# Kernel tuning notes

Hardware: AMD Instinct MI355X
Metric: run time of the kernel (lower is better)

Reference implementation:

```python
import math
import jax, jax.numpy as jnp
import numpy as np

# dims: batch, in-channels, out-channels, features (freq bins), frames, heads, expansion
B, C, CO, F, W, NH, EXP = 1, 8, 8, 512, 256, 8, 4
CC = C + CO          # channels into cross-attn query (cat of h and self_attn)
FC = C + 2 * CO      # channels into FFN (cat of h, self_attn, src_attn)
FH = F * EXP         # FFN hidden features


def mc_linear(x, pw, dw=None):
    # x: [B,Cin,Fin,W]; pw: [Cin,Fout,Fin] per-channel positionwise matmul;
    # dw: [Cout,Cin] channel-mixing matmul ('depthwise' in the repo's naming)
    y = jnp.einsum('bcfw,cgf->bcgw', x, pw)
    if dw is not None:
        y = jnp.einsum('bcgw,oc->bogw', y, dw)
    return y


def frame_conv(x, w, b):
    # Conv2d kernel (1,3), padding (0,1): 1D conv along the frame axis
    y = jax.lax.conv_general_dilated(x, w, (1, 1), ((0, 0), (1, 1)),
                                     dimension_numbers=('NCHW', 'OIHW', 'NCHW'))
    return y + b[None, :, None, None]


def mc_layernorm(x, g, b, eps=1e-5):
    # normalize over the feature axis (2), per (batch, channel, frame)
    mu = x.mean(axis=2, keepdims=True)
    var = jnp.mean(jnp.square(x - mu), axis=2, keepdims=True)
    return (x - mu) * jax.lax.rsqrt(var + eps) * g[None, :, :, None] + b[None, :, :, None]


def mc_attention(xq, xkv, q_pw, q_dw, q_cw, q_cb, k_pw, k_cw, k_cb, v_pw, v_cw, v_cb, o_pw):
    q = frame_conv(mc_linear(xq, q_pw, q_dw), q_cw, q_cb)   # [B,CO,F,Wq]
    k = frame_conv(mc_linear(xkv, k_pw), k_cw, k_cb)        # [B,CO,F,Wk]
    v = frame_conv(mc_linear(xkv, v_pw), v_cw, v_cb)
    dh = F // NH

    def heads(t):  # [B,CO,F,Wt] -> [B,CO,NH,Wt,dh]
        b_, c_, f_, w_ = t.shape
        return t.transpose(0, 1, 3, 2).reshape(b_, c_, w_, NH, dh).transpose(0, 1, 3, 2, 4)

    qh, kh, vh = heads(q), heads(k), heads(v)
    qk = jnp.einsum('bchqd,bchkd->bchqk', qh, kh) / math.sqrt(F)
    a = jnp.einsum('bchqk,bchkd->bchqd', jax.nn.softmax(qk, axis=-1), vh)
    b_, c_, h_, w_, _ = a.shape
    a = a.transpose(0, 1, 3, 2, 4).reshape(b_, c_, w_, F).transpose(0, 1, 3, 2)  # [B,CO,F,Wq]
    return mc_linear(a, o_pw), qk


def setup_inputs() -> dict:
    key = jax.random.key(0)
    ks = jax.random.split(key, 32)
    it = iter(range(32))

    def rn(shape, s=0.02):
        return jax.random.normal(ks[next(it)], shape, jnp.float32) * s

    inp = {
        'x': jax.random.normal(ks[next(it)], (B, C, F, W), jnp.float32),
        'src': jax.random.normal(ks[next(it)], (B, C, F, W), jnp.float32),
        'ln_g': jnp.ones((C, F), jnp.float32),
        'ln_b': jnp.zeros((C, F), jnp.float32),
        # self-attention (C -> CO, C == CO so no channel-mix on projections)
        'sa_q_pw': rn((C, F, F)), 'sa_q_cw': rn((CO, CO, 1, 3), 0.1), 'sa_q_cb': jnp.zeros((CO,), jnp.float32),
        'sa_k_pw': rn((C, F, F)), 'sa_k_cw': rn((CO, CO, 1, 3), 0.1), 'sa_k_cb': jnp.zeros((CO,), jnp.float32),
        'sa_v_pw': rn((C, F, F)), 'sa_v_cw': rn((CO, CO, 1, 3), 0.1), 'sa_v_cb': jnp.zeros((CO,), jnp.float32),
        'sa_o_pw': rn((CO, F, F)),
        # cross-attention (query from CC=C+CO channels -> CO; key/value from src with C channels)
        'ca_q_pw': rn((CC, F, F)), 'ca_q_dw': rn((CO, CC), 0.1),
        'ca_q_cw': rn((CO, CO, 1, 3), 0.1), 'ca_q_cb': jnp.zeros((CO,), jnp.float32),
        'ca_k_pw': rn((C, F, F)), 'ca_k_cw': rn((CO, CO, 1, 3), 0.1), 'ca_k_cb': jnp.zeros((CO,), jnp.float32),
        'ca_v_pw': rn((C, F, F)), 'ca_v_cw': rn((CO, CO, 1, 3), 0.1), 'ca_v_cb': jnp.zeros((CO,), jnp.float32),
        'ca_o_pw': rn((CO, F, F)),
        # FFN
        'ffn1_pw': rn((FC, FH, F)), 'ffn1_dw': rn((FC, FC), 0.1),
        'ffn2_pw': rn((FC, F, FH)), 'ffn2_dw': rn((C, FC), 0.1),
    }
    return inp


def reference(x, src, ln_g, ln_b,
              sa_q_pw, sa_q_cw, sa_q_cb, sa_k_pw, sa_k_cw, sa_k_cb, sa_v_pw, sa_v_cw, sa_v_cb, sa_o_pw,
              ca_q_pw, ca_q_dw, ca_q_cw, ca_q_cb, ca_k_pw, ca_k_cw, ca_k_cb, ca_v_pw, ca_v_cw, ca_v_cb, ca_o_pw,
              ffn1_pw, ffn1_dw, ffn2_pw, ffn2_dw):
    h = mc_layernorm(x, ln_g, ln_b)
    sa, qk1 = mc_attention(h, h, sa_q_pw, None, sa_q_cw, sa_q_cb,
                           sa_k_pw, sa_k_cw, sa_k_cb, sa_v_pw, sa_v_cw, sa_v_cb, sa_o_pw)
    ca, qk2 = mc_attention(jnp.concatenate([h, sa], axis=1), src,
                           ca_q_pw, ca_q_dw, ca_q_cw, ca_q_cb,
                           ca_k_pw, ca_k_cw, ca_k_cb, ca_v_pw, ca_v_cw, ca_v_cb, ca_o_pw)
    z = mc_linear(jnp.concatenate([h, sa, ca], axis=1), ffn1_pw, ffn1_dw)
    z = jax.nn.gelu(z, approximate=False)
    z = mc_linear(z, ffn2_pw, ffn2_dw)
    return (x + z, qk1, qk2)
```

## Files before the change

### kernel.cpp

```cpp
#include <hip/hip_runtime.h>
#include <math.h>

typedef __attribute__((ext_vector_type(4))) float f32x4;
typedef __attribute__((ext_vector_type(8))) short s16x8;
typedef __attribute__((ext_vector_type(4))) short s16x4;

__device__ __forceinline__ unsigned short f2b(float f) {
    union { float f; unsigned u; } v; v.f = f;
    unsigned r = v.u + 0x7fffu + ((v.u >> 16) & 1u);
    return (unsigned short)(r >> 16);
}
__device__ __forceinline__ float b2f(unsigned short u) {
    union { unsigned u; float f; } v; v.u = ((unsigned)u) << 16;
    return v.f;
}

constexpr int kF = 512;
constexpr int kW = 256;
constexpr int kFW = kF * kW;

__global__ __launch_bounds__(256) void ln_t_kernel(const float* __restrict__ x,
                                                   const float* __restrict__ g,
                                                   const float* __restrict__ b,
                                                   unsigned short* __restrict__ hTb) {
    int c = blockIdx.x >> 4;
    int w0 = (blockIdx.x & 15) * 16;
    int t = threadIdx.x;
    int wi = t & 15, fg = t >> 4;
    const float* xb = x + (size_t)c * kFW + w0 + wi;
    float sum = 0.f, sum2 = 0.f;
    for (int j = 0; j < 32; ++j) {
        float v = xb[(size_t)(fg * 32 + j) * kW];
        sum += v; sum2 += v * v;
    }
    __shared__ float s1[16][16], s2[16][16];
    s1[fg][wi] = sum; s2[fg][wi] = sum2;
    __syncthreads();
    float ts = 0.f, tq = 0.f;
    #pragma unroll
    for (int j = 0; j < 16; ++j) { ts += s1[j][wi]; tq += s2[j][wi]; }
    float mu = ts * (1.0f / 512.0f);
    float rstd = rsqrtf(tq * (1.0f / 512.0f) - mu * mu + 1e-5f);
    const float* gc = g + c * kF + fg * 32;
    const float* bc = b + c * kF + fg * 32;
    unsigned short* ob = hTb + (size_t)c * kFW + (size_t)(w0 + wi) * kF + fg * 32;
    for (int j = 0; j < 32; j += 4) {
        float v0 = xb[(size_t)(fg * 32 + j + 0) * kW];
        float v1 = xb[(size_t)(fg * 32 + j + 1) * kW];
        float v2 = xb[(size_t)(fg * 32 + j + 2) * kW];
        float v3 = xb[(size_t)(fg * 32 + j + 3) * kW];
        s16x4 p = { (short)f2b((v0 - mu) * rstd * gc[j + 0] + bc[j + 0]),
                    (short)f2b((v1 - mu) * rstd * gc[j + 1] + bc[j + 1]),
                    (short)f2b((v2 - mu) * rstd * gc[j + 2] + bc[j + 2]),
                    (short)f2b((v3 - mu) * rstd * gc[j + 3] + bc[j + 3]) };
        *(s16x4*)(&ob[j]) = p;
    }
}

__global__ __launch_bounds__(256) void tcvt_kernel(const float* __restrict__ in,
                                                   unsigned short* __restrict__ out) {
    int c = blockIdx.x, f0 = blockIdx.y * 64, w0 = blockIdx.z * 64;
    __shared__ float tile[64][65];
    int t = threadIdx.x;
    int tw = t & 63, tf4 = t >> 6;
    for (int i = 0; i < 16; ++i) {
        int f = tf4 * 16 + i;
        tile[f][tw] = in[(size_t)c * kFW + (size_t)(f0 + f) * kW + w0 + tw];
    }
    __syncthreads();
    int w = t >> 2, fc = (t & 3) * 16;
    unsigned short* ob = out + (size_t)c * kFW + (size_t)(w0 + w) * kF + f0 + fc;
    for (int j = 0; j < 16; j += 4) {
        s16x4 p = { (short)f2b(tile[fc + j + 0][w]), (short)f2b(tile[fc + j + 1][w]),
                    (short)f2b(tile[fc + j + 2][w]), (short)f2b(tile[fc + j + 3][w]) };
        *(s16x4*)(&ob[j]) = p;
    }
}

struct WSeg { const float* A; const unsigned short* B; void* C; int omode; };
struct WB5 { WSeg s[5]; };

__global__ __launch_bounds__(256) void wgemm256(WB5 wb, int M, int K, int Klocal,
                                                long a_ch, long b_ch, long c_ch, long c_split,
                                                int segshift, int nm, int ksplit) {
    __shared__ unsigned short lds[16384];
    int t = threadIdx.x, lane = t & 63, wv = t >> 6;
    int l16 = lane & 15, l4 = lane >> 4;

    int id = blockIdx.x;
    int r = id & 7, j = id >> 3;
    int per = nm * ksplit;
    int y = r + 8 * (j / per);
    int rem = j % per;
    int mt = rem % nm;
    int kz = rem / nm;
    int seg = y >> segshift, c = y & ((1 << segshift) - 1);
    WSeg sg = wb.s[seg];
    int bm = mt * 64;
    int kbase = kz * Klocal;

    const float* A = sg.A + (size_t)c * a_ch + kbase;
    const unsigned short* B = sg.B + (size_t)c * b_ch + kbase;
    const float* arow = A + (size_t)(bm + wv * 16 + l16) * K + l4 * 8;

    int srow = t >> 3, sck = t & 7;
    const unsigned short* bsrc = B + (size_t)srow * K + sck * 8;
    unsigned short* sdst = &lds[srow * 64 + ((sck * 8) ^ ((srow & 7) << 3))];

    s16x8 stg0, stg1, stg2, stg3, stg4, stg5, stg6, stg7;
    #define LOADSTG(c0) do { \
        const unsigned short* _b = bsrc + (size_t)(c0) * 64; \
        stg0 = *(const s16x8*)(_b); \
        stg1 = *(const s16x8*)(_b + (size_t)32 * K); \
        stg2 = *(const s16x8*)(_b + (size_t)64 * K); \
        stg3 = *(const s16x8*)(_b + (size_t)96 * K); \
        stg4 = *(const s16x8*)(_b + (size_t)128 * K); \
        stg5 = *(const s16x8*)(_b + (size_t)160 * K); \
        stg6 = *(const s16x8*)(_b + (size_t)192 * K); \
        stg7 = *(const s16x8*)(_b + (size_t)224 * K); \
    } while (0)
    #define WRITESTG() do { \
        *(s16x8*)(&sdst[0])     = stg0; \
        *(s16x8*)(&sdst[2048])  = stg1; \
        *(s16x8*)(&sdst[4096])  = stg2; \
        *(s16x8*)(&sdst[6144])  = stg3; \
        *(s16x8*)(&sdst[8192])  = stg4; \
        *(s16x8*)(&sdst[10240]) = stg5; \
        *(s16x8*)(&sdst[12288]) = stg6; \
        *(s16x8*)(&sdst[14336]) = stg7; \
    } while (0)

    f32x4 acc[16];
    #pragma unroll
    for (int i = 0; i < 16; ++i) acc[i] = (f32x4){0.f, 0.f, 0.f, 0.f};

    LOADSTG(0);
    WRITESTG();

    f32x4 pa0 = __builtin_nontemporal_load((const f32x4*)arow);
    f32x4 pa1 = __builtin_nontemporal_load((const f32x4*)(arow + 4));

    int nc = Klocal >> 6;
    for (int cch = 0; cch < nc; ++cch) {
        __syncthreads();
        if (cch + 1 < nc) LOADSTG(cch + 1);
        #pragma unroll
        for (int ks = 0; ks < 2; ++ks) {
            f32x4 c0 = pa0, c1 = pa1;
            int nk = cch * 64 + (ks + 1) * 32;
            if (nk < Klocal) {
                pa0 = __builtin_nontemporal_load((const f32x4*)(arow + nk));
                pa1 = __builtin_nontemporal_load((const f32x4*)(arow + nk + 4));
            }
            s16x8 af = { (short)f2b(c0.x), (short)f2b(c0.y), (short)f2b(c0.z), (short)f2b(c0.w),
                         (short)f2b(c1.x), (short)f2b(c1.y), (short)f2b(c1.z), (short)f2b(c1.w) };
            #pragma unroll
            for (int ni = 0; ni < 16; ++ni) {
                int rr = ni * 16 + l16;
                s16x8 bf = *(const s16x8*)(&lds[rr * 64 + (((ks * 32 + l4 * 8)) ^ ((rr & 7) << 3))]);
                acc[ni] = __builtin_amdgcn_mfma_f32_16x16x32_bf16(af, bf, acc[ni], 0, 0, 0);
            }
        }
        __syncthreads();
        if (cch + 1 < nc) WRITESTG();
    }
    #undef LOADSTG
    #undef WRITESTG

    int m0 = bm + wv * 16 + l4 * 4;
    if (sg.omode == 2) {
        unsigned short* C = (unsigned short*)sg.C + (size_t)c * c_ch;
        #pragma unroll
        for (int ni = 0; ni < 16; ++ni) {
            int n = ni * 16 + l16;
            s16x4 pk = { (short)f2b(acc[ni][0]), (short)f2b(acc[ni][1]),
                         (short)f2b(acc[ni][2]), (short)f2b(acc[ni][3]) };
            *(s16x4*)(&C[(size_t)n * M + m0]) = pk;
        }
    } else if (sg.omode == 1) {
        unsigned short* C = (unsigned short*)sg.C + (size_t)c * c_ch;
        #pragma unroll
        for (int ni = 0; ni < 16; ++ni) {
            int n = ni * 16 + l16;
            #pragma unroll
            for (int rr = 0; rr < 4; ++rr)
                C[(size_t)(m0 + rr) * 256 + n] = f2b(acc[ni][rr]);
        }
    } else {
        float* C = (float*)sg.C + (size_t)c * c_ch + (size_t)kz * c_split;
        #pragma unroll
        for (int ni = 0; ni < 16; ++ni) {
            int n = ni * 16 + l16;
            #pragma unroll
            for (int rr = 0; rr < 4; ++rr)
                C[(size_t)(m0 + rr) * 256 + n] = acc[ni][rr];
        }
    }
}

template<int OMODE, int BN>
__global__ __launch_bounds__(256) void gemm_mfma(
    const unsigned short* __restrict__ Av, const unsigned short* __restrict__ B,
    void* __restrict__ Cv,
    int M, int N, int K,
    long a_hi, long a_lo, long b_hi, long b_lo, long c_hi, long c_lo,
    int bshift, int a_rs, int b_rs, int c_rs, float scale)
{
    constexpr int NF = BN / 64;
    constexpr int WN = BN / 4;
    __shared__ unsigned char lds[8192 + BN * 128];

    int t = threadIdx.x;
    int lane = t & 63, wv = t >> 6;
    int l16 = lane & 15, l4 = lane >> 4;
    int swz = (lane & 7) << 4;

    int by = blockIdx.y;
    int bhi = by >> bshift, blo = by & ((1 << bshift) - 1);
    int ntiles = N / BN;
    int bm = (blockIdx.x / ntiles) * 64;
    int bn = (blockIdx.x % ntiles) * BN;

    const unsigned short* Bp = B + (size_t)bhi * b_hi + (size_t)blo * b_lo + (size_t)bn * b_rs;
    const unsigned short* A = Av + (size_t)bhi * a_hi + (size_t)blo * a_lo;

    f32x4 acc[4][NF];
    #pragma unroll
    for (int i = 0; i < 4; ++i)
        #pragma unroll
        for (int j = 0; j < NF; ++j) acc[i][j] = (f32x4){0.f, 0.f, 0.f, 0.f};

    for (int k0 = 0; k0 < K; k0 += 64) {
        #pragma unroll
        for (int it = 0; it < 2; ++it) {
            int idx = it * 256 + t;
            int rr = idx >> 3, ck = idx & 7;
            s16x8 v = *(const s16x8*)(A + (size_t)(bm + rr) * a_rs + k0 + ck * 8);
            int off = rr * 128 + ((ck * 16) ^ ((rr & 7) << 4));
            *(s16x8*)(&lds[off]) = v;
        }
        #pragma unroll
        for (int it = 0; it < BN / 32; ++it) {
            int idx = it * 256 + t;
            int rr = idx >> 3, ck = idx & 7;
            s16x8 v = *(const s16x8*)(Bp + (size_t)rr * b_rs + k0 + ck * 8);
            int off = 8192 + rr * 128 + ((ck * 16) ^ ((rr & 7) << 4));
            *(s16x8*)(&lds[off]) = v;
        }
        __syncthreads();
        #pragma unroll
        for (int ks = 0; ks < 2; ++ks) {
            s16x8 af[4], bfr[NF];
            #pragma unroll
            for (int mi = 0; mi < 4; ++mi)
                af[mi] = *(const s16x8*)(&lds[(mi * 16 + l16) * 128 + ((ks * 64 + l4 * 16) ^ swz)]);
            #pragma unroll
            for (int ni = 0; ni < NF; ++ni)
                bfr[ni] = *(const s16x8*)(&lds[8192 + (wv * WN + ni * 16 + l16) * 128 + ((ks * 64 + l4 * 16) ^ swz)]);
            #pragma unroll
            for (int mi = 0; mi < 4; ++mi)
                #pragma unroll
                for (int ni = 0; ni < NF; ++ni)
                    acc[mi][ni] = __builtin_amdgcn_mfma_f32_16x16x32_bf16(af[mi], bfr[ni], acc[mi][ni], 0, 0, 0);
        }
        __syncthreads();
    }

    unsigned short* C = (unsigned short*)Cv + (size_t)bhi * c_hi + (size_t)blo * c_lo;
    #pragma unroll
    for (int mi = 0; mi < 4; ++mi)
        #pragma unroll
        for (int ni = 0; ni < NF; ++ni) {
            int n = bn + wv * WN + ni * 16 + l16;
            int m0 = bm + mi * 16 + l4 * 4;
            #pragma unroll
            for (int rr = 0; rr < 4; ++rr)
                C[(size_t)(m0 + rr) * c_rs + n] = f2b(acc[mi][ni][rr] * scale);
        }
}

struct ConvArgs {
    const unsigned short* in[5];
    unsigned short* out[5];
    const float* cw[5];
    const float* cb[5];
    int mode[5];
};

__global__ __launch_bounds__(256) void conv5_kernel(ConvArgs a) {
    int g = blockIdx.y;
    __shared__ float scw[192]; __shared__ float scb[8];
    int t = threadIdx.x;
    if (t < 192) scw[t] = a.cw[g][t];
    if (t >= 192 && t < 200) scb[t - 192] = a.cb[g][t - 192];
    __syncthreads();
    const unsigned short* in = a.in[g];
    unsigned short* out = a.out[g];
    int gi = blockIdx.x * 256 + t;
    int mode = a.mode[g];
    int w = mode ? (gi & 255) : (gi >> 9);
    int str = mode ? 1 : 512;
    float acc[8];
    #pragma unroll
    for (int o = 0; o < 8; ++o) acc[o] = scb[o];
    bool hm = w > 0, hp = w < 255;
    #pragma unroll
    for (int i = 0; i < 8; ++i) {
        size_t base = (size_t)i * kFW + gi;
        float xm = hm ? b2f(in[base - str]) : 0.f;
        float x0 = b2f(in[base]);
        float xp = hp ? b2f(in[base + str]) : 0.f;
        #pragma unroll
        for (int o = 0; o < 8; ++o) {
            const float* wp = &scw[(o * 8 + i) * 3];
            acc[o] += wp[0] * xm + wp[1] * x0 + wp[2] * xp;
        }
    }
    #pragma unroll
    for (int o = 0; o < 8; ++o) out[(size_t)o * kFW + gi] = f2b(acc[o]);
}

__global__ __launch_bounds__(256) void mixconv_kernel(const unsigned short* __restrict__ in,
                                                      const float* __restrict__ dw,
                                                      const float* __restrict__ cw,
                                                      const float* __restrict__ cb,
                                                      unsigned short* __restrict__ out) {
    __shared__ float sdw[128], scw[192], scb[8];
    int t = threadIdx.x;
    if (t < 128) sdw[t] = dw[t];
    if (t >= 128 && t < 136) scb[t - 128] = cb[t - 128];
    if (t < 192) scw[t] = cw[t];
    __syncthreads();
    int gi = blockIdx.x * 256 + t;
    int w = gi >> 9;
    bool hm = w > 0, hp = w < 255;
    float xc[16], xm[16], xp[16];
    #pragma unroll
    for (int cc = 0; cc < 16; ++cc) {
        size_t base = (size_t)cc * kFW + gi;
        xc[cc] = b2f(in[base]);
        xm[cc] = hm ? b2f(in[base - 512]) : 0.f;
        xp[cc] = hp ? b2f(in[base + 512]) : 0.f;
    }
    float mm[8], m0[8], mp[8];
    #pragma unroll
    for (int o = 0; o < 8; ++o) {
        float am = 0.f, a0 = 0.f, ap = 0.f;
        #pragma unroll
        for (int cc = 0; cc < 16; ++cc) {
            float wv = sdw[o * 16 + cc];
            am += wv * xm[cc]; a0 += wv * xc[cc]; ap += wv * xp[cc];
        }
        mm[o] = am; m0[o] = a0; mp[o] = ap;
    }
    #pragma unroll
    for (int o = 0; o < 8; ++o) {
        float acc = scb[o];
        #pragma unroll
        for (int i = 0; i < 8; ++i) {
            const float* wp = &scw[(o * 8 + i) * 3];
            acc += wp[0] * mm[i] + wp[1] * m0[i] + wp[2] * mp[i];
        }
        out[(size_t)o * kFW + gi] = f2b(acc);
    }
}

__global__ __launch_bounds__(256) void qk_softmax_kernel(
    const unsigned short* __restrict__ Qt, const unsigned short* __restrict__ Kt,
    float* __restrict__ S, unsigned short* __restrict__ P, float scale)
{
    __shared__ unsigned char lds[40960];
    __shared__ float smax[4][64];
    __shared__ float ssum[4][64];
    int t = threadIdx.x, lane = t & 63, wv = t >> 6;
    int l16 = lane & 15, l4 = lane >> 4;
    int swz = (lane & 7) << 4;
    int ch = blockIdx.y, c = ch >> 3, h = ch & 7;
    int bm = blockIdx.x * 64;
    const unsigned short* Qb = Qt + (size_t)c * kFW + h * 64;
    const unsigned short* Kb = Kt + (size_t)c * kFW + h * 64;
    float* Sb = S + (size_t)ch * 65536;
    unsigned short* Pb = P + (size_t)ch * 65536;

    #pragma unroll
    for (int it = 0; it < 2; ++it) {
        int idx = it * 256 + t; int rr = idx >> 3, ck = idx & 7;
        s16x8 v = *(const s16x8*)(Qb + (size_t)(bm + rr) * 512 + ck * 8);
        *(s16x8*)(&lds[rr * 128 + ((ck * 16) ^ ((rr & 7) << 4))]) = v;
    }
    #pragma unroll
    for (int it = 0; it < 8; ++it) {
        int idx = it * 256 + t; int rr = idx >> 3, ck = idx & 7;
        s16x8 v = *(const s16x8*)(Kb + (size_t)rr * 512 + ck * 8);
        *(s16x8*)(&lds[8192 + rr * 128 + ((ck * 16) ^ ((rr & 7) << 4))]) = v;
    }
    __syncthreads();
    f32x4 acc[4][4];
    #pragma unroll
    for (int i = 0; i < 4; ++i)
        #pragma unroll
        for (int j = 0; j < 4; ++j) acc[i][j] = (f32x4){0.f, 0.f, 0.f, 0.f};
    #pragma unroll
    for (int ks = 0; ks < 2; ++ks) {
        s16x8 af[4], bfr[4];
        #pragma unroll
        for (int mi = 0; mi < 4; ++mi)
            af[mi] = *(const s16x8*)(&lds[(mi * 16 + l16) * 128 + ((ks * 64 + l4 * 16) ^ swz)]);
        #pragma unroll
        for (int ni = 0; ni < 4; ++ni)
            bfr[ni] = *(const s16x8*)(&lds[8192 + (wv * 64 + ni * 16 + l16) * 128 + ((ks * 64 + l4 * 16) ^ swz)]);
        #pragma unroll
        for (int mi = 0; mi < 4; ++mi)
            #pragma unroll
            for (int ni = 0; ni < 4; ++ni)
                acc[mi][ni] = __builtin_amdgcn_mfma_f32_16x16x32_bf16(af[mi], bfr[ni], acc[mi][ni], 0, 0, 0);
    }
    #pragma unroll
    for (int mi = 0; mi < 4; ++mi)
        #pragma unroll
        for (int ni = 0; ni < 4; ++ni) {
            acc[mi][ni] *= scale;
            int col = wv * 64 + ni * 16 + l16;
            int row0 = bm + mi * 16 + l4 * 4;
            #pragma unroll
            for (int rr = 0; rr < 4; ++rr)
                Sb[(size_t)(row0 + rr) * 256 + col] = acc[mi][ni][rr];
        }
    float rmax[4][4];
    #pragma unroll
    for (int mi = 0; mi < 4; ++mi)
        #pragma unroll
        for (int rr = 0; rr < 4; ++rr)
            rmax[mi][rr] = fmaxf(fmaxf(acc[mi][0][rr], acc[mi][1][rr]), fmaxf(acc[mi][2][rr], acc[mi][3][rr]));
    #pragma unroll
    for (int d = 1; d < 16; d <<= 1)
        #pragma unroll
        for (int mi = 0; mi < 4; ++mi)
            #pragma unroll
            for (int rr = 0; rr < 4; ++rr)
                rmax[mi][rr] = fmaxf(rmax[mi][rr], __shfl_xor(rmax[mi][rr], d));
    if (l16 == 0)
        #pragma unroll
        for (int mi = 0; mi < 4; ++mi)
            #pragma unroll
            for (int rr = 0; rr < 4; ++rr)
                smax[wv][mi * 16 + l4 * 4 + rr] = rmax[mi][rr];
    __syncthreads();
    float rM[4][4], rsum[4][4];
    #pragma unroll
    for (int mi = 0; mi < 4; ++mi)
        #pragma unroll
        for (int rr = 0; rr < 4; ++rr) {
            int row = mi * 16 + l4 * 4 + rr;
            rM[mi][rr] = fmaxf(fmaxf(smax[0][row], smax[1][row]), fmaxf(smax[2][row], smax[3][row]));
            rsum[mi][rr] = 0.f;
        }
    #pragma unroll
    for (int mi = 0; mi < 4; ++mi)
        #pragma unroll
        for (int ni = 0; ni < 4; ++ni)
            #pragma unroll
            for (int rr = 0; rr < 4; ++rr) {
                float e = __expf(acc[mi][ni][rr] - rM[mi][rr]);
                acc[mi][ni][rr] = e;
                rsum[mi][rr] += e;
            }
    #pragma unroll
    for (int d = 1; d < 16; d <<= 1)
        #pragma unroll
        for (int mi = 0; mi < 4; ++mi)
            #pragma unroll
            for (int rr = 0; rr < 4; ++rr)
                rsum[mi][rr] += __shfl_xor(rsum[mi][rr], d);
    if (l16 == 0)
        #pragma unroll
        for (int mi = 0; mi < 4; ++mi)
            #pragma unroll
            for (int rr = 0; rr < 4; ++rr)
                ssum[wv][mi * 16 + l4 * 4 + rr] = rsum[mi][rr];
    __syncthreads();
    #pragma unroll
    for (int mi = 0; mi < 4; ++mi)
        #pragma unroll
        for (int rr = 0; rr < 4; ++rr) {
            int row = mi * 16 + l4 * 4 + rr;
            float inv = 1.f / (ssum[0][row] + ssum[1][row] + ssum[2][row] + ssum[3][row]);
            #pragma unroll
            for (int ni = 0; ni < 4; ++ni)
                Pb[(size_t)(bm + row) * 256 + wv * 64 + ni * 16 + l16] = f2b(acc[mi][ni][rr] * inv);
        }
}

__global__ __launch_bounds__(256) void gelu24_kernel(unsigned short* __restrict__ z,
                                                     const float* __restrict__ dw) {
    __shared__ float sdw[576];
    int t = threadIdx.x;
    for (int i = t; i < 576; i += 256) sdw[i] = dw[i];
    __syncthreads();
    size_t gi = (size_t)blockIdx.x * 256 + t;
    const size_t CH = (size_t)256 * 2048;
    float xv[24];
    #pragma unroll
    for (int cc = 0; cc < 24; ++cc) xv[cc] = b2f(z[cc * CH + gi]);
    #pragma unroll
    for (int o = 0; o < 24; ++o) {
        float s = 0.f;
        #pragma unroll
        for (int cc = 0; cc < 24; ++cc) s += sdw[o * 24 + cc] * xv[cc];
        s = 0.5f * s * (1.0f + erff(s * 0.7071067811865475f));
        z[o * CH + gi] = f2b(s);
    }
}

__global__ __launch_bounds__(256) void final_mix_add2(const float* __restrict__ x,
                                                      const float* __restrict__ z2,
                                                      const float* __restrict__ dw,
                                                      float* __restrict__ out) {
    __shared__ float sdw[192];
    int t = threadIdx.x;
    if (t < 192) sdw[t] = dw[t];
    __syncthreads();
    int gi = blockIdx.x * 256 + t;
    const size_t PSZ = (size_t)24 * kFW;
    float xv[24];
    #pragma unroll
    for (int cc = 0; cc < 24; ++cc) {
        size_t o = (size_t)cc * kFW + gi;
        xv[cc] = z2[o] + z2[PSZ + o];
    }
    #pragma unroll
    for (int o = 0; o < 8; ++o) {
        float s = 0.f;
        #pragma unroll
        for (int cc = 0; cc < 24; ++cc) s += sdw[o * 24 + cc] * xv[cc];
        out[(size_t)o * kFW + gi] = x[(size_t)o * kFW + gi] + s;
    }
}

extern "C" void kernel_launch(void* const* d_in, const int* in_sizes, int n_in,
                              void* d_out, int out_size, void* d_ws, size_t ws_size,
                              hipStream_t stream) {
    const float* x       = (const float*)d_in[0];
    const float* src     = (const float*)d_in[1];
    const float* ln_g    = (const float*)d_in[2];
    const float* ln_b    = (const float*)d_in[3];
    const float* sa_q_pw = (const float*)d_in[4];
    const float* sa_q_cw = (const float*)d_in[5];
    const float* sa_q_cb = (const float*)d_in[6];
    const float* sa_k_pw = (const float*)d_in[7];
    const float* sa_k_cw = (const float*)d_in[8];
    const float* sa_k_cb = (const float*)d_in[9];
    const float* sa_v_pw = (const float*)d_in[10];
    const float* sa_v_cw = (const float*)d_in[11];
    const float* sa_v_cb = (const float*)d_in[12];
    const float* sa_o_pw = (const float*)d_in[13];
    const float* ca_q_pw = (const float*)d_in[14];
    const float* ca_q_dw = (const float*)d_in[15];
    const float* ca_q_cw = (const float*)d_in[16];
    const float* ca_q_cb = (const float*)d_in[17];
    const float* ca_k_pw = (const float*)d_in[18];
    const float* ca_k_cw = (const float*)d_in[19];
    const float* ca_k_cb = (const float*)d_in[20];
    const float* ca_v_pw = (const float*)d_in[21];
    const float* ca_v_cw = (const float*)d_in[22];
    const float* ca_v_cb = (const float*)d_in[23];
    const float* ca_o_pw = (const float*)d_in[24];
    const float* ffn1_pw = (const float*)d_in[25];
    const float* ffn1_dw = (const float*)d_in[26];
    const float* ffn2_pw = (const float*)d_in[27];
    const float* ffn2_dw = (const float*)d_in[28];

    float* out  = (float*)d_out;
    float* qk1o = out + 1048576;
    float* qk2o = out + 1048576 + 4194304;

    unsigned char* ws = (unsigned char*)d_ws;
    unsigned short* CAT24  = (unsigned short*)(ws + 0);
    unsigned short* hTb    = CAT24;
    unsigned short* saTb   = CAT24 + 8 * (size_t)kFW;
    unsigned short* caTb   = CAT24 + 16 * (size_t)kFW;
    unsigned short* SRCT   = (unsigned short*)(ws + 6291456);
    unsigned short* preQ   = (unsigned short*)(ws + 8388608);
    unsigned short* preK   = (unsigned short*)(ws + 10485760);
    unsigned short* preVsa = (unsigned short*)(ws + 12582912);
    unsigned short* preKca = (unsigned short*)(ws + 14680064);
    unsigned short* preVca = (unsigned short*)(ws + 16777216);
    unsigned short* QT     = (unsigned short*)(ws + 18874368);
    unsigned short* KT     = (unsigned short*)(ws + 20971520);
    unsigned short* VNsa   = (unsigned short*)(ws + 23068672);
    unsigned short* KTca   = (unsigned short*)(ws + 25165824);
    unsigned short* VNca   = (unsigned short*)(ws + 27262976);
    unsigned short* PRE16  = (unsigned short*)(ws + 29360128);
    unsigned short* QTca   = (unsigned short*)(ws + 33554432);
    unsigned short* ATTT   = (unsigned short*)(ws + 35651584);
    unsigned short* PB     = (unsigned short*)(ws + 37748736);
    unsigned short* Z0T    = (unsigned short*)(ws + 8388608);
    float*          Z2P    = (float*)(ws + 33554432);

    const float qscale = 0.044194173824159216f;
    dim3 blk(256);

    ln_t_kernel<<<128, blk, 0, stream>>>(x, ln_g, ln_b, hTb);
    tcvt_kernel<<<dim3(8, 8, 4), blk, 0, stream>>>(src, SRCT);

    WB5 p5;
    p5.s[0] = { sa_q_pw, hTb,  preQ,   2 };
    p5.s[1] = { sa_k_pw, hTb,  preK,   2 };
    p5.s[2] = { sa_v_pw, hTb,  preVsa, 1 };
    p5.s[3] = { ca_k_pw, SRCT, preKca, 2 };
    p5.s[4] = { ca_v_pw, SRCT, preVca, 1 };
    wgemm256<<<dim3(320), blk, 0, stream>>>(p5, 512, 512, 512, 262144, kFW, kFW, 0, 3, 8, 1);

    ConvArgs c5;
    c5.in[0] = preQ;   c5.out[0] = QT;   c5.cw[0] = sa_q_cw; c5.cb[0] = sa_q_cb; c5.mode[0] = 0;
    c5.in[1] = preK;   c5.out[1] = KT;   c5.cw[1] = sa_k_cw; c5.cb[1] = sa_k_cb; c5.mode[1] = 0;
    c5.in[2] = preVsa; c5.out[2] = VNsa; c5.cw[2] = sa_v_cw; c5.cb[2] = sa_v_cb; c5.mode[2] = 1;
    c5.in[3] = preKca; c5.out[3] = KTca; c5.cw[3] = ca_k_cw; c5.cb[3] = ca_k_cb; c5.mode[3] = 0;
    c5.in[4] = preVca; c5.out[4] = VNca; c5.cw[4] = ca_v_cw; c5.cb[4] = ca_v_cb; c5.mode[4] = 1;
    conv5_kernel<<<dim3(512, 5), blk, 0, stream>>>(c5);

    qk_softmax_kernel<<<dim3(4, 64), blk, 0, stream>>>(QT, KT, qk1o, PB, qscale);
    gemm_mfma<1, 64><<<dim3(4, 64), blk, 0, stream>>>(PB, VNsa, ATTT, 256, 64, 256,
        524288, 65536, kFW, 16384, kFW, 64, 3, 256, 256, 512, 1.0f);
    WB5 so;
    so.s[0] = { sa_o_pw, ATTT, saTb, 2 };
    so.s[1] = so.s[0]; so.s[2] = so.s[0]; so.s[3] = so.s[0]; so.s[4] = so.s[0];
    wgemm256<<<dim3(64), blk, 0, stream>>>(so, 512, 512, 512, 262144, kFW, kFW, 0, 8, 8, 1);

    WB5 cq;
    cq.s[0] = { ca_q_pw, CAT24, PRE16, 2 };
    cq.s[1] = cq.s[0]; cq.s[2] = cq.s[0]; cq.s[3] = cq.s[0]; cq.s[4] = cq.s[0];
    wgemm256<<<dim3(128), blk, 0, stream>>>(cq, 512, 512, 512, 262144, kFW, kFW, 0, 8, 8, 1);
    mixconv_kernel<<<512, blk, 0, stream>>>(PRE16, ca_q_dw, ca_q_cw, ca_q_cb, QTca);

    qk_softmax_kernel<<<dim3(4, 64), blk, 0, stream>>>(QTca, KTca, qk2o, PB, qscale);
    gemm_mfma<1, 64><<<dim3(4, 64), blk, 0, stream>>>(PB, VNca, ATTT, 256, 64, 256,
        524288, 65536, kFW, 16384, kFW, 64, 3, 256, 256, 512, 1.0f);
    WB5 co;
    co.s[0] = { ca_o_pw, ATTT, caTb, 2 };
    co.s[1] = co.s[0]; co.s[2] = co.s[0]; co.s[3] = co.s[0]; co.s[4] = co.s[0];
    wgemm256<<<dim3(64), blk, 0, stream>>>(co, 512, 512, 512, 262144, kFW, kFW, 0, 8, 8, 1);

    WB5 f1;
    f1.s[0] = { ffn1_pw, CAT24, Z0T, 2 };
    f1.s[1] = f1.s[0]; f1.s[2] = f1.s[0]; f1.s[3] = f1.s[0]; f1.s[4] = f1.s[0];
    wgemm256<<<dim3(768), blk, 0, stream>>>(f1, 2048, 512, 512, 1048576, kFW, 524288, 0, 8, 32, 1);
    gelu24_kernel<<<2048, blk, 0, stream>>>(Z0T, ffn1_dw);
    WB5 f2;
    f2.s[0] = { ffn2_pw, Z0T, Z2P, 0 };
    f2.s[1] = f2.s[0]; f2.s[2] = f2.s[0]; f2.s[3] = f2.s[0]; f2.s[4] = f2.s[0];
    wgemm256<<<dim3(384), blk, 0, stream>>>(f2, 512, 2048, 1024, 1048576, 524288, kFW, 3145728, 8, 8, 2);
    final_mix_add2<<<512, blk, 0, stream>>>(x, Z2P, ffn2_dw, out);
}
```

Measured before the change: 288.4 us.

## Fuse attention kernels, double-buffer weight GEMM, merge prep and early cross-attn Q projection

Combines several changes. LayerNorm and the src transpose now run in one prep launch. The weight GEMM gets double-buffered LDS with A-operand prefetch. QK-softmax and PV are fused into one attention kernel, so the probability matrix no longer round-trips through global memory. The h-part of the cross-attention Q projection moves into the first batched GEMM, so only the sa-part runs later. This cuts launches and intermediate traffic but doubles GEMM LDS usage, which may lower occupancy.

```diff
diff --git a/kernel.cpp b/kernel.cpp
--- a/kernel.cpp
+++ b/kernel.cpp
@@ -19,71 +19,95 @@
 constexpr int kW = 256;
 constexpr int kFW = kF * kW;
 
-__global__ __launch_bounds__(256) void ln_t_kernel(const float* __restrict__ x,
+__global__ __launch_bounds__(256) void prep_kernel(const float* __restrict__ x,
                                                    const float* __restrict__ g,
                                                    const float* __restrict__ b,
-                                                   unsigned short* __restrict__ hTb) {
-    int c = blockIdx.x >> 4;
-    int w0 = (blockIdx.x & 15) * 16;
+                                                   unsigned short* __restrict__ hTb,
+                                                   const float* __restrict__ src,
+                                                   unsigned short* __restrict__ SRCT) {
+    __shared__ float tile[64][65];
+    __shared__ float s1[16][16], s2[16][16];
+    int bid = blockIdx.x;
     int t = threadIdx.x;
-    int wi = t & 15, fg = t >> 4;
-    const float* xb = x + (size_t)c * kFW + w0 + wi;
-    float sum = 0.f, sum2 = 0.f;
-    for (int j = 0; j < 32; ++j) {
-        float v = xb[(size_t)(fg * 32 + j) * kW];
-        sum += v; sum2 += v * v;
-    }
-    __shared__ float s1[16][16], s2[16][16];
-    s1[fg][wi] = sum; s2[fg][wi] = sum2;
-    __syncthreads();
-    float ts = 0.f, tq = 0.f;
-    #pragma unroll
-    for (int j = 0; j < 16; ++j) { ts += s1[j][wi]; tq += s2[j][wi]; }
-    float mu = ts * (1.0f / 512.0f);
-    float rstd = rsqrtf(tq * (1.0f / 512.0f) - mu * mu + 1e-5f);
-    const float* gc = g + c * kF + fg * 32;
-    const float* bc = b + c * kF + fg * 32;
-    unsigned short* ob = hTb + (size_t)c * kFW + (size_t)(w0 + wi) * kF + fg * 32;
-    for (int j = 0; j < 32; j += 4) {
-        float v0 = xb[(size_t)(fg * 32 + j + 0) * kW];
-        float v1 = xb[(size_t)(fg * 32 + j + 1) * kW];
-        float v2 = xb[(size_t)(fg * 32 + j + 2) * kW];
-        float v3 = xb[(size_t)(fg * 32 + j + 3) * kW];
-        s16x4 p = { (short)f2b((v0 - mu) * rstd * gc[j + 0] + bc[j + 0]),
-                    (short)f2b((v1 - mu) * rstd * gc[j + 1] + bc[j + 1]),
-                    (short)f2b((v2 - mu) * rstd * gc[j + 2] + bc[j + 2]),
-                    (short)f2b((v3 - mu) * rstd * gc[j + 3] + bc[j + 3]) };
-        *(s16x4*)(&ob[j]) = p;
-    }
-}
-
-__global__ __launch_bounds__(256) void tcvt_kernel(const float* __restrict__ in,
-                                                   unsigned short* __restrict__ out) {
-    int c = blockIdx.x, f0 = blockIdx.y * 64, w0 = blockIdx.z * 64;
-    __shared__ float tile[64][65];
-    int t = threadIdx.x;
-    int tw = t & 63, tf4 = t >> 6;
-    for (int i = 0; i < 16; ++i) {
-        int f = tf4 * 16 + i;
-        tile[f][tw] = in[(size_t)c * kFW + (size_t)(f0 + f) * kW + w0 + tw];
-    }
-    __syncthreads();
-    int w = t >> 2, fc = (t & 3) * 16;
-    unsigned short* ob = out + (size_t)c * kFW + (size_t)(w0 + w) * kF + f0 + fc;
-    for (int j = 0; j < 16; j += 4) {
-        s16x4 p = { (short)f2b(tile[fc + j + 0][w]), (short)f2b(tile[fc + j + 1][w]),
-                    (short)f2b(tile[fc + j + 2][w]), (short)f2b(tile[fc + j + 3][w]) };
-        *(s16x4*)(&ob[j]) = p;
+    if (bid < 128) {
+        int c = bid >> 4;
+        int w0 = (bid & 15) * 16;
+        int wi = t & 15, fg = t >> 4;
+        const float* xb = x + (size_t)c * kFW + w0 + wi;
+        float sum = 0.f, sum2 = 0.f;
+        for (int j = 0; j < 32; ++j) {
+            float v = xb[(size_t)(fg * 32 + j) * kW];
+            sum += v; sum2 += v * v;
+        }
+        s1[fg][wi] = sum; s2[fg][wi] = sum2;
+        __syncthreads();
+        float ts = 0.f, tq = 0.f;
+        #pragma unroll
+        for (int j = 0; j < 16; ++j) { ts += s1[j][wi]; tq += s2[j][wi]; }
+        float mu = ts * (1.0f / 512.0f);
+        float rstd = rsqrtf(tq * (1.0f / 512.0f) - mu * mu + 1e-5f);
+        const float* gc = g + c * kF + fg * 32;
+        const float* bc = b + c * kF + fg * 32;
+        unsigned short* ob = hTb + (size_t)c * kFW + (size_t)(w0 + wi) * kF + fg * 32;
+        for (int j = 0; j < 32; j += 4) {
+            float v0 = xb[(size_t)(fg * 32 + j + 0) * kW];
+            float v1 = xb[(size_t)(fg * 32 + j + 1) * kW];
+            float v2 = xb[(size_t)(fg * 32 + j + 2) * kW];
+            float v3 = xb[(size_t)(fg * 32 + j + 3) * kW];
+            s16x4 p = { (short)f2b((v0 - mu) * rstd * gc[j + 0] + bc[j + 0]),
+                        (short)f2b((v1 - mu) * rstd * gc[j + 1] + bc[j + 1]),
+                        (short)f2b((v2 - mu) * rstd * gc[j + 2] + bc[j + 2]),
+                        (short)f2b((v3 - mu) * rstd * gc[j + 3] + bc[j + 3]) };
+            *(s16x4*)(&ob[j]) = p;
+        }
+    } else {
+        int fid = bid - 128;
+        int c = fid >> 5;
+        int f0 = ((fid >> 2) & 7) * 64, w0 = (fid & 3) * 64;
+        int tw = t & 63, tf4 = t >> 6;
+        for (int i = 0; i < 16; ++i) {
+            int f = tf4 * 16 + i;
+            tile[f][tw] = src[(size_t)c * kFW + (size_t)(f0 + f) * kW + w0 + tw];
+        }
+        __syncthreads();
+        int w = t >> 2, fc = (t & 3) * 16;
+        unsigned short* ob = SRCT + (size_t)c * kFW + (size_t)(w0 + w) * kF + f0 + fc;
+        for (int j = 0; j < 16; j += 4) {
+            s16x4 p = { (short)f2b(tile[fc + j + 0][w]), (short)f2b(tile[fc + j + 1][w]),
+                        (short)f2b(tile[fc + j + 2][w]), (short)f2b(tile[fc + j + 3][w]) };
+            *(s16x4*)(&ob[j]) = p;
+        }
     }
 }
 
 struct WSeg { const float* A; const unsigned short* B; void* C; int omode; };
-struct WB5 { WSeg s[5]; };
-
-__global__ __launch_bounds__(256) void wgemm256(WB5 wb, int M, int K, int Klocal,
+struct WB8 { WSeg s[8]; };
+
+__device__ __forceinline__ void wg_compute(const unsigned short* __restrict__ ldsbuf,
+                                           f32x4 A0, f32x4 A1, f32x4 A2, f32x4 A3,
+                                           f32x4* acc, int l16, int l4) {
+    s16x8 af0 = { (short)f2b(A0.x), (short)f2b(A0.y), (short)f2b(A0.z), (short)f2b(A0.w),
+                  (short)f2b(A1.x), (short)f2b(A1.y), (short)f2b(A1.z), (short)f2b(A1.w) };
+    #pragma unroll
+    for (int ni = 0; ni < 16; ++ni) {
+        int rr = ni * 16 + l16;
+        s16x8 bf = *(const s16x8*)(&ldsbuf[rr * 64 + ((l4 * 8) ^ ((rr & 7) << 3))]);
+        acc[ni] = __builtin_amdgcn_mfma_f32_16x16x32_bf16(af0, bf, acc[ni], 0, 0, 0);
+    }
+    s16x8 af1 = { (short)f2b(A2.x), (short)f2b(A2.y), (short)f2b(A2.z), (short)f2b(A2.w),
+                  (short)f2b(A3.x), (short)f2b(A3.y), (short)f2b(A3.z), (short)f2b(A3.w) };
+    #pragma unroll
+    for (int ni = 0; ni < 16; ++ni) {
+        int rr = ni * 16 + l16;
+        s16x8 bf = *(const s16x8*)(&ldsbuf[rr * 64 + ((32 + l4 * 8) ^ ((rr & 7) << 3))]);
+        acc[ni] = __builtin_amdgcn_mfma_f32_16x16x32_bf16(af1, bf, acc[ni], 0, 0, 0);
+    }
+}
+
+__global__ __launch_bounds__(256) void wgemm256(WB8 wb, int M, int K, int Klocal,
                                                 long a_ch, long b_ch, long c_ch, long c_split,
                                                 int segshift, int nm, int ksplit) {
-    __shared__ unsigned short lds[16384];
+    __shared__ unsigned short lds[2][16384];
     int t = threadIdx.x, lane = t & 63, wv = t >> 6;
     int l16 = lane & 15, l4 = lane >> 4;
 
@@ -105,11 +129,12 @@
 
     int srow = t >> 3, sck = t & 7;
     const unsigned short* bsrc = B + (size_t)srow * K + sck * 8;
-    unsigned short* sdst = &lds[srow * 64 + ((sck * 8) ^ ((srow & 7) << 3))];
+    int sdoff = srow * 64 + ((sck * 8) ^ ((srow & 7) << 3));
 
     s16x8 stg0, stg1, stg2, stg3, stg4, stg5, stg6, stg7;
-    #define LOADSTG(c0) do { \
-        const unsigned short* _b = bsrc + (size_t)(c0) * 64; \
+    f32x4 a0, a1, a2, a3, e0, e1, e2, e3;
+
+    #define LOADSTG(c0) do { const unsigned short* _b = bsrc + (size_t)(c0) * 64; \
         stg0 = *(const s16x8*)(_b); \
         stg1 = *(const s16x8*)(_b + (size_t)32 * K); \
         stg2 = *(const s16x8*)(_b + (size_t)64 * K); \
@@ -117,55 +142,43 @@
         stg4 = *(const s16x8*)(_b + (size_t)128 * K); \
         stg5 = *(const s16x8*)(_b + (size_t)160 * K); \
         stg6 = *(const s16x8*)(_b + (size_t)192 * K); \
-        stg7 = *(const s16x8*)(_b + (size_t)224 * K); \
-    } while (0)
-    #define WRITESTG() do { \
-        *(s16x8*)(&sdst[0])     = stg0; \
-        *(s16x8*)(&sdst[2048])  = stg1; \
-        *(s16x8*)(&sdst[4096])  = stg2; \
-        *(s16x8*)(&sdst[6144])  = stg3; \
-        *(s16x8*)(&sdst[8192])  = stg4; \
-        *(s16x8*)(&sdst[10240]) = stg5; \
-        *(s16x8*)(&sdst[12288]) = stg6; \
-        *(s16x8*)(&sdst[14336]) = stg7; \
-    } while (0)
+        stg7 = *(const s16x8*)(_b + (size_t)224 * K); } while (0)
+    #define WRITESTG(bi) do { unsigned short* _d = &lds[bi][sdoff]; \
+        *(s16x8*)(_d + 0)     = stg0; \
+        *(s16x8*)(_d + 2048)  = stg1; \
+        *(s16x8*)(_d + 4096)  = stg2; \
+        *(s16x8*)(_d + 6144)  = stg3; \
+        *(s16x8*)(_d + 8192)  = stg4; \
+        *(s16x8*)(_d + 10240) = stg5; \
+        *(s16x8*)(_d + 12288) = stg6; \
+        *(s16x8*)(_d + 14336) = stg7; } while (0)
+    #define LDA(d0,d1,d2,d3,koff) do { \
+        d0 = __builtin_nontemporal_load((const f32x4*)(arow + (koff))); \
+        d1 = __builtin_nontemporal_load((const f32x4*)(arow + (koff) + 4)); \
+        d2 = __builtin_nontemporal_load((const f32x4*)(arow + (koff) + 32)); \
+        d3 = __builtin_nontemporal_load((const f32x4*)(arow + (koff) + 36)); } while (0)
 
     f32x4 acc[16];
     #pragma unroll
     for (int i = 0; i < 16; ++i) acc[i] = (f32x4){0.f, 0.f, 0.f, 0.f};
 
-    LOADSTG(0);
-    WRITESTG();
-
-    f32x4 pa0 = __builtin_nontemporal_load((const f32x4*)arow);
-    f32x4 pa1 = __builtin_nontemporal_load((const f32x4*)(arow + 4));
+    LOADSTG(0); LDA(a0, a1, a2, a3, 0);
+    WRITESTG(0);
 
     int nc = Klocal >> 6;
-    for (int cch = 0; cch < nc; ++cch) {
+    for (int cch = 0; cch < nc; cch += 2) {
+        LOADSTG(cch + 1); LDA(e0, e1, e2, e3, (cch + 1) * 64);
         __syncthreads();
-        if (cch + 1 < nc) LOADSTG(cch + 1);
-        #pragma unroll
-        for (int ks = 0; ks < 2; ++ks) {
-            f32x4 c0 = pa0, c1 = pa1;
-            int nk = cch * 64 + (ks + 1) * 32;
-            if (nk < Klocal) {
-                pa0 = __builtin_nontemporal_load((const f32x4*)(arow + nk));
-                pa1 = __builtin_nontemporal_load((const f32x4*)(arow + nk + 4));
-            }
-            s16x8 af = { (short)f2b(c0.x), (short)f2b(c0.y), (short)f2b(c0.z), (short)f2b(c0.w),
-                         (short)f2b(c1.x), (short)f2b(c1.y), (short)f2b(c1.z), (short)f2b(c1.w) };
-            #pragma unroll
-            for (int ni = 0; ni < 16; ++ni) {
-                int rr = ni * 16 + l16;
-                s16x8 bf = *(const s16x8*)(&lds[rr * 64 + (((ks * 32 + l4 * 8)) ^ ((rr & 7) << 3))]);
-                acc[ni] = __builtin_amdgcn_mfma_f32_16x16x32_bf16(af, bf, acc[ni], 0, 0, 0);
-            }
-        }
+        wg_compute(lds[0], a0, a1, a2, a3, acc, l16, l4);
+        WRITESTG(1);
+        if (cch + 2 < nc) { LOADSTG(cch + 2); LDA(a0, a1, a2, a3, (cch + 2) * 64); }
         __syncthreads();
-        if (cch + 1 < nc) WRITESTG();
+        wg_compute(lds[1], e0, e1, e2, e3, acc, l16, l4);
+        if (cch + 2 < nc) WRITESTG(0);
     }
     #undef LOADSTG
     #undef WRITESTG
+    #undef LDA
 
     int m0 = bm + wv * 16 + l4 * 4;
     if (sg.omode == 2) {
@@ -198,85 +211,183 @@
     }
 }
 
-template<int OMODE, int BN>
-__global__ __launch_bounds__(256) void gemm_mfma(
-    const unsigned short* __restrict__ Av, const unsigned short* __restrict__ B,
-    void* __restrict__ Cv,
-    int M, int N, int K,
-    long a_hi, long a_lo, long b_hi, long b_lo, long c_hi, long c_lo,
-    int bshift, int a_rs, int b_rs, int c_rs, float scale)
+__global__ __launch_bounds__(256) void attn_kernel(
+    const unsigned short* __restrict__ Qt, const unsigned short* __restrict__ Kt,
+    const unsigned short* __restrict__ VN, float* __restrict__ S,
+    unsigned short* __restrict__ ATTT, float scale)
 {
-    constexpr int NF = BN / 64;
-    constexpr int WN = BN / 4;
-    __shared__ unsigned char lds[8192 + BN * 128];
-
-    int t = threadIdx.x;
-    int lane = t & 63, wv = t >> 6;
+    __shared__ unsigned short q_lds[4096];
+    __shared__ unsigned short kv_lds[16384];
+    __shared__ unsigned short p_lds[16384];
+    __shared__ float smax[4][64], ssum[4][64], sinv[64];
+    int t = threadIdx.x, lane = t & 63, wv = t >> 6;
     int l16 = lane & 15, l4 = lane >> 4;
-    int swz = (lane & 7) << 4;
-
-    int by = blockIdx.y;
-    int bhi = by >> bshift, blo = by & ((1 << bshift) - 1);
-    int ntiles = N / BN;
-    int bm = (blockIdx.x / ntiles) * 64;
-    int bn = (blockIdx.x % ntiles) * BN;
-
-    const unsigned short* Bp = B + (size_t)bhi * b_hi + (size_t)blo * b_lo + (size_t)bn * b_rs;
-    const unsigned short* A = Av + (size_t)bhi * a_hi + (size_t)blo * a_lo;
-
-    f32x4 acc[4][NF];
+    int ch = blockIdx.y, c = ch >> 3, h = ch & 7;
+    int bm = blockIdx.x * 64;
+    const unsigned short* Qb = Qt + (size_t)c * kFW + h * 64;
+    const unsigned short* Kb = Kt + (size_t)c * kFW + h * 64;
+    const unsigned short* Vb = VN + (size_t)c * kFW + (size_t)(h * 64) * 256;
+    float* Sb = S + (size_t)ch * 65536;
+    unsigned short* Ab = ATTT + (size_t)c * kFW + h * 64;
+
+    s16x8 qr[2], kr[8], vr[8];
+    #pragma unroll
+    for (int i = 0; i < 2; ++i) {
+        int idx = i * 256 + t; int rr = idx >> 3, ck = idx & 7;
+        qr[i] = *(const s16x8*)(Qb + (size_t)(bm + rr) * 512 + ck * 8);
+    }
+    #pragma unroll
+    for (int i = 0; i < 8; ++i) {
+        int idx = i * 256 + t; int rr = idx >> 3, ck = idx & 7;
+        kr[i] = *(const s16x8*)(Kb + (size_t)rr * 512 + ck * 8);
+    }
+    #pragma unroll
+    for (int i = 0; i < 8; ++i) {
+        int idx = i * 256 + t; int d = idx >> 5, cs = idx & 31;
+        vr[i] = *(const s16x8*)(Vb + (size_t)d * 256 + cs * 8);
+    }
+    #pragma unroll
+    for (int i = 0; i < 2; ++i) {
+        int idx = i * 256 + t; int rr = idx >> 3, ck = idx & 7;
+        *(s16x8*)(&q_lds[rr * 64 + ((ck * 8) ^ ((rr & 7) << 3))]) = qr[i];
+    }
+    #pragma unroll
+    for (int i = 0; i < 8; ++i) {
+        int idx = i * 256 + t; int rr = idx >> 3, ck = idx & 7;
+        *(s16x8*)(&kv_lds[rr * 64 + ((ck * 8) ^ ((rr & 7) << 3))]) = kr[i];
+    }
+    __syncthreads();
+
+    f32x4 acc[4][4];
     #pragma unroll
     for (int i = 0; i < 4; ++i)
         #pragma unroll
-        for (int j = 0; j < NF; ++j) acc[i][j] = (f32x4){0.f, 0.f, 0.f, 0.f};
-
-    for (int k0 = 0; k0 < K; k0 += 64) {
-        #pragma unroll
-        for (int it = 0; it < 2; ++it) {
-            int idx = it * 256 + t;
-            int rr = idx >> 3, ck = idx & 7;
-            s16x8 v = *(const s16x8*)(A + (size_t)(bm + rr) * a_rs + k0 + ck * 8);
-            int off = rr * 128 + ((ck * 16) ^ ((rr & 7) << 4));
-            *(s16x8*)(&lds[off]) = v;
-        }
-        #pragma unroll
-        for (int it = 0; it < BN / 32; ++it) {
-            int idx = it * 256 + t;
-            int rr = idx >> 3, ck = idx & 7;
-            s16x8 v = *(const s16x8*)(Bp + (size_t)rr * b_rs + k0 + ck * 8);
-            int off = 8192 + rr * 128 + ((ck * 16) ^ ((rr & 7) << 4));
-            *(s16x8*)(&lds[off]) = v;
-        }
-        __syncthreads();
-        #pragma unroll
-        for (int ks = 0; ks < 2; ++ks) {
-            s16x8 af[4], bfr[NF];
-            #pragma unroll
-            for (int mi = 0; mi < 4; ++mi)
-                af[mi] = *(const s16x8*)(&lds[(mi * 16 + l16) * 128 + ((ks * 64 + l4 * 16) ^ swz)]);
-            #pragma unroll
-            for (int ni = 0; ni < NF; ++ni)
-                bfr[ni] = *(const s16x8*)(&lds[8192 + (wv * WN + ni * 16 + l16) * 128 + ((ks * 64 + l4 * 16) ^ swz)]);
-            #pragma unroll
-            for (int mi = 0; mi < 4; ++mi)
-                #pragma unroll
-                for (int ni = 0; ni < NF; ++ni)
-                    acc[mi][ni] = __builtin_amdgcn_mfma_f32_16x16x32_bf16(af[mi], bfr[ni], acc[mi][ni], 0, 0, 0);
-        }
-        __syncthreads();
-    }
-
-    unsigned short* C = (unsigned short*)Cv + (size_t)bhi * c_hi + (size_t)blo * c_lo;
+        for (int jj = 0; jj < 4; ++jj) acc[i][jj] = (f32x4){0.f, 0.f, 0.f, 0.f};
+    #pragma unroll
+    for (int ks = 0; ks < 2; ++ks) {
+        s16x8 af[4], bfr[4];
+        #pragma unroll
+        for (int mi = 0; mi < 4; ++mi) {
+            int rq = mi * 16 + l16;
+            af[mi] = *(const s16x8*)(&q_lds[rq * 64 + ((ks * 32 + l4 * 8) ^ ((rq & 7) << 3))]);
+        }
+        #pragma unroll
+        for (int ni = 0; ni < 4; ++ni) {
+            int rk = wv * 64 + ni * 16 + l16;
+            bfr[ni] = *(const s16x8*)(&kv_lds[rk * 64 + ((ks * 32 + l4 * 8) ^ ((rk & 7) << 3))]);
+        }
+        #pragma unroll
+        for (int mi = 0; mi < 4; ++mi)
+            #pragma unroll
+            for (int ni = 0; ni < 4; ++ni)
+                acc[mi][ni] = __builtin_amdgcn_mfma_f32_16x16x32_bf16(af[mi], bfr[ni], acc[mi][ni], 0, 0, 0);
+    }
+
     #pragma unroll
     for (int mi = 0; mi < 4; ++mi)
         #pragma unroll
-        for (int ni = 0; ni < NF; ++ni) {
-            int n = bn + wv * WN + ni * 16 + l16;
-            int m0 = bm + mi * 16 + l4 * 4;
+        for (int ni = 0; ni < 4; ++ni) {
+            acc[mi][ni] *= scale;
+            int col = wv * 64 + ni * 16 + l16;
+            int row0 = bm + mi * 16 + l4 * 4;
             #pragma unroll
             for (int rr = 0; rr < 4; ++rr)
-                C[(size_t)(m0 + rr) * c_rs + n] = f2b(acc[mi][ni][rr] * scale);
-        }
+                Sb[(size_t)(row0 + rr) * 256 + col] = acc[mi][ni][rr];
+        }
+
+    float rmax[4][4];
+    #pragma unroll
+    for (int mi = 0; mi < 4; ++mi)
+        #pragma unroll
+        for (int rr = 0; rr < 4; ++rr)
+            rmax[mi][rr] = fmaxf(fmaxf(acc[mi][0][rr], acc[mi][1][rr]), fmaxf(acc[mi][2][rr], acc[mi][3][rr]));
+    #pragma unroll
+    for (int d = 1; d < 16; d <<= 1)
+        #pragma unroll
+        for (int mi = 0; mi < 4; ++mi)
+            #pragma unroll
+            for (int rr = 0; rr < 4; ++rr)
+                rmax[mi][rr] = fmaxf(rmax[mi][rr], __shfl_xor(rmax[mi][rr], d));
+    if (l16 == 0)
+        #pragma unroll
+        for (int mi = 0; mi < 4; ++mi)
+            #pragma unroll
+            for (int rr = 0; rr < 4; ++rr)
+                smax[wv][mi * 16 + l4 * 4 + rr] = rmax[mi][rr];
+    __syncthreads();
+    float rsum[4][4];
+    #pragma unroll
+    for (int mi = 0; mi < 4; ++mi)
+        #pragma unroll
+        for (int rr = 0; rr < 4; ++rr) {
+            int row = mi * 16 + l4 * 4 + rr;
+            float rM = fmaxf(fmaxf(smax[0][row], smax[1][row]), fmaxf(smax[2][row], smax[3][row]));
+            rsum[mi][rr] = 0.f;
+            #pragma unroll
+            for (int ni = 0; ni < 4; ++ni) {
+                float e = __expf(acc[mi][ni][rr] - rM);
+                acc[mi][ni][rr] = e;
+                rsum[mi][rr] += e;
+            }
+        }
+    #pragma unroll
+    for (int d = 1; d < 16; d <<= 1)
+        #pragma unroll
+        for (int mi = 0; mi < 4; ++mi)
+            #pragma unroll
+            for (int rr = 0; rr < 4; ++rr)
+                rsum[mi][rr] += __shfl_xor(rsum[mi][rr], d);
+    if (l16 == 0)
+        #pragma unroll
+        for (int mi = 0; mi < 4; ++mi)
+            #pragma unroll
+            for (int rr = 0; rr < 4; ++rr)
+                ssum[wv][mi * 16 + l4 * 4 + rr] = rsum[mi][rr];
+    __syncthreads();
+
+    #pragma unroll
+    for (int i = 0; i < 8; ++i) {
+        int idx = i * 256 + t; int d = idx >> 5, cs = idx & 31;
+        *(s16x8*)(&kv_lds[d * 256 + ((cs * 8) ^ ((d & 7) << 3))]) = vr[i];
+    }
+    #pragma unroll
+    for (int mi = 0; mi < 4; ++mi)
+        #pragma unroll
+        for (int ni = 0; ni < 4; ++ni) {
+            int col = wv * 64 + ni * 16 + l16;
+            int cb = col & ~7, cl = col & 7;
+            #pragma unroll
+            for (int rr = 0; rr < 4; ++rr) {
+                int row = mi * 16 + l4 * 4 + rr;
+                p_lds[row * 256 + (cb ^ ((row & 7) << 3)) + cl] = f2b(acc[mi][ni][rr]);
+            }
+        }
+    if (t < 64) sinv[t] = 1.f / (ssum[0][t] + ssum[1][t] + ssum[2][t] + ssum[3][t]);
+    __syncthreads();
+
+    f32x4 po[4];
+    #pragma unroll
+    for (int ni = 0; ni < 4; ++ni) po[ni] = (f32x4){0.f, 0.f, 0.f, 0.f};
+    int qrow = wv * 16 + l16;
+    #pragma unroll
+    for (int ks = 0; ks < 8; ++ks) {
+        s16x8 paf = *(const s16x8*)(&p_lds[qrow * 256 + ((ks * 32 + l4 * 8) ^ ((qrow & 7) << 3))]);
+        #pragma unroll
+        for (int ni = 0; ni < 4; ++ni) {
+            int rd = ni * 16 + l16;
+            s16x8 bf = *(const s16x8*)(&kv_lds[rd * 256 + ((ks * 32 + l4 * 8) ^ ((rd & 7) << 3))]);
+            po[ni] = __builtin_amdgcn_mfma_f32_16x16x32_bf16(paf, bf, po[ni], 0, 0, 0);
+        }
+    }
+    #pragma unroll
+    for (int ni = 0; ni < 4; ++ni) {
+        int d = ni * 16 + l16;
+        #pragma unroll
+        for (int rr = 0; rr < 4; ++rr) {
+            int row = wv * 16 + l4 * 4 + rr;
+            Ab[(size_t)(bm + row) * 512 + d] = f2b(po[ni][rr] * sinv[row]);
+        }
+    }
 }
 
 struct ConvArgs {
@@ -363,132 +474,6 @@
         }
         out[(size_t)o * kFW + gi] = f2b(acc);
     }
-}
-
-__global__ __launch_bounds__(256) void qk_softmax_kernel(
-    const unsigned short* __restrict__ Qt, const unsigned short* __restrict__ Kt,
-    float* __restrict__ S, unsigned short* __restrict__ P, float scale)
-{
-    __shared__ unsigned char lds[40960];
-    __shared__ float smax[4][64];
-    __shared__ float ssum[4][64];
-    int t = threadIdx.x, lane = t & 63, wv = t >> 6;
-    int l16 = lane & 15, l4 = lane >> 4;
-    int swz = (lane & 7) << 4;
-    int ch = blockIdx.y, c = ch >> 3, h = ch & 7;
-    int bm = blockIdx.x * 64;
-    const unsigned short* Qb = Qt + (size_t)c * kFW + h * 64;
-    const unsigned short* Kb = Kt + (size_t)c * kFW + h * 64;
-    float* Sb = S + (size_t)ch * 65536;
-    unsigned short* Pb = P + (size_t)ch * 65536;
-
-    #pragma unroll
-    for (int it = 0; it < 2; ++it) {
-        int idx = it * 256 + t; int rr = idx >> 3, ck = idx & 7;
-        s16x8 v = *(const s16x8*)(Qb + (size_t)(bm + rr) * 512 + ck * 8);
-        *(s16x8*)(&lds[rr * 128 + ((ck * 16) ^ ((rr & 7) << 4))]) = v;
-    }
-    #pragma unroll
-    for (int it = 0; it < 8; ++it) {
-        int idx = it * 256 + t; int rr = idx >> 3, ck = idx & 7;
-        s16x8 v = *(const s16x8*)(Kb + (size_t)rr * 512 + ck * 8);
-        *(s16x8*)(&lds[8192 + rr * 128 + ((ck * 16) ^ ((rr & 7) << 4))]) = v;
-    }
-    __syncthreads();
-    f32x4 acc[4][4];
-    #pragma unroll
-    for (int i = 0; i < 4; ++i)
-        #pragma unroll
-        for (int j = 0; j < 4; ++j) acc[i][j] = (f32x4){0.f, 0.f, 0.f, 0.f};
-    #pragma unroll
-    for (int ks = 0; ks < 2; ++ks) {
-        s16x8 af[4], bfr[4];
-        #pragma unroll
-        for (int mi = 0; mi < 4; ++mi)
-            af[mi] = *(const s16x8*)(&lds[(mi * 16 + l16) * 128 + ((ks * 64 + l4 * 16) ^ swz)]);
-        #pragma unroll
-        for (int ni = 0; ni < 4; ++ni)
-            bfr[ni] = *(const s16x8*)(&lds[8192 + (wv * 64 + ni * 16 + l16) * 128 + ((ks * 64 + l4 * 16) ^ swz)]);
-        #pragma unroll
-        for (int mi = 0; mi < 4; ++mi)
-            #pragma unroll
-            for (int ni = 0; ni < 4; ++ni)
-                acc[mi][ni] = __builtin_amdgcn_mfma_f32_16x16x32_bf16(af[mi], bfr[ni], acc[mi][ni], 0, 0, 0);
-    }
-    #pragma unroll
-    for (int mi = 0; mi < 4; ++mi)
-        #pragma unroll
-        for (int ni = 0; ni < 4; ++ni) {
-            acc[mi][ni] *= scale;
-            int col = wv * 64 + ni * 16 + l16;
-            int row0 = bm + mi * 16 + l4 * 4;
-            #pragma unroll
-            for (int rr = 0; rr < 4; ++rr)
-                Sb[(size_t)(row0 + rr) * 256 + col] = acc[mi][ni][rr];
-        }
-    float rmax[4][4];
-    #pragma unroll
-    for (int mi = 0; mi < 4; ++mi)
-        #pragma unroll
-        for (int rr = 0; rr < 4; ++rr)
-            rmax[mi][rr] = fmaxf(fmaxf(acc[mi][0][rr], acc[mi][1][rr]), fmaxf(acc[mi][2][rr], acc[mi][3][rr]));
-    #pragma unroll
-    for (int d = 1; d < 16; d <<= 1)
-        #pragma unroll
-        for (int mi = 0; mi < 4; ++mi)
-            #pragma unroll
-            for (int rr = 0; rr < 4; ++rr)
-                rmax[mi][rr] = fmaxf(rmax[mi][rr], __shfl_xor(rmax[mi][rr], d));
-    if (l16 == 0)
-        #pragma unroll
-        for (int mi = 0; mi < 4; ++mi)
-            #pragma unroll
-            for (int rr = 0; rr < 4; ++rr)
-                smax[wv][mi * 16 + l4 * 4 + rr] = rmax[mi][rr];
-    __syncthreads();
-    float rM[4][4], rsum[4][4];
-    #pragma unroll
-    for (int mi = 0; mi < 4; ++mi)
-        #pragma unroll
-        for (int rr = 0; rr < 4; ++rr) {
-            int row = mi * 16 + l4 * 4 + rr;
-            rM[mi][rr] = fmaxf(fmaxf(smax[0][row], smax[1][row]), fmaxf(smax[2][row], smax[3][row]));
-            rsum[mi][rr] = 0.f;
-        }
-    #pragma unroll
-    for (int mi = 0; mi < 4; ++mi)
-        #pragma unroll
-        for (int ni = 0; ni < 4; ++ni)
-            #pragma unroll
-            for (int rr = 0; rr < 4; ++rr) {
-                float e = __expf(acc[mi][ni][rr] - rM[mi][rr]);
-                acc[mi][ni][rr] = e;
-                rsum[mi][rr] += e;
-            }
-    #pragma unroll
-    for (int d = 1; d < 16; d <<= 1)
-        #pragma unroll
-        for (int mi = 0; mi < 4; ++mi)
-            #pragma unroll
-            for (int rr = 0; rr < 4; ++rr)
-                rsum[mi][rr] += __shfl_xor(rsum[mi][rr], d);
-    if (l16 == 0)
-        #pragma unroll
-        for (int mi = 0; mi < 4; ++mi)
-            #pragma unroll
-            for (int rr = 0; rr < 4; ++rr)
-                ssum[wv][mi * 16 + l4 * 4 + rr] = rsum[mi][rr];
-    __syncthreads();
-    #pragma unroll
-    for (int mi = 0; mi < 4; ++mi)
-        #pragma unroll
-        for (int rr = 0; rr < 4; ++rr) {
-            int row = mi * 16 + l4 * 4 + rr;
-            float inv = 1.f / (ssum[0][row] + ssum[1][row] + ssum[2][row] + ssum[3][row]);
-            #pragma unroll
-            for (int ni = 0; ni < 4; ++ni)
-                Pb[(size_t)(bm + row) * 256 + wv * 64 + ni * 16 + l16] = f2b(acc[mi][ni][rr] * inv);
-        }
 }
 
 __global__ __launch_bounds__(256) void gelu24_kernel(unsigned short* __restrict__ z,
@@ -593,23 +578,23 @@
     unsigned short* PRE16  = (unsigned short*)(ws + 29360128);
     unsigned short* QTca   = (unsigned short*)(ws + 33554432);
     unsigned short* ATTT   = (unsigned short*)(ws + 35651584);
-    unsigned short* PB     = (unsigned short*)(ws + 37748736);
     unsigned short* Z0T    = (unsigned short*)(ws + 8388608);
-    float*          Z2P    = (float*)(ws + 33554432);
+    float*          Z2P    = (float*)(ws + 37748736);
 
     const float qscale = 0.044194173824159216f;
     dim3 blk(256);
 
-    ln_t_kernel<<<128, blk, 0, stream>>>(x, ln_g, ln_b, hTb);
-    tcvt_kernel<<<dim3(8, 8, 4), blk, 0, stream>>>(src, SRCT);
-
-    WB5 p5;
-    p5.s[0] = { sa_q_pw, hTb,  preQ,   2 };
-    p5.s[1] = { sa_k_pw, hTb,  preK,   2 };
-    p5.s[2] = { sa_v_pw, hTb,  preVsa, 1 };
-    p5.s[3] = { ca_k_pw, SRCT, preKca, 2 };
-    p5.s[4] = { ca_v_pw, SRCT, preVca, 1 };
-    wgemm256<<<dim3(320), blk, 0, stream>>>(p5, 512, 512, 512, 262144, kFW, kFW, 0, 3, 8, 1);
+    prep_kernel<<<384, blk, 0, stream>>>(x, ln_g, ln_b, hTb, src, SRCT);
+
+    WB8 p6;
+    p6.s[0] = { sa_q_pw, hTb,  preQ,   2 };
+    p6.s[1] = { sa_k_pw, hTb,  preK,   2 };
+    p6.s[2] = { sa_v_pw, hTb,  preVsa, 1 };
+    p6.s[3] = { ca_k_pw, SRCT, preKca, 2 };
+    p6.s[4] = { ca_v_pw, SRCT, preVca, 1 };
+    p6.s[5] = { ca_q_pw, hTb,  PRE16,  2 };
+    p6.s[6] = p6.s[0]; p6.s[7] = p6.s[0];
+    wgemm256<<<dim3(384), blk, 0, stream>>>(p6, 512, 512, 512, 262144, kFW, kFW, 0, 3, 8, 1);
 
     ConvArgs c5;
     c5.in[0] = preQ;   c5.out[0] = QT;   c5.cw[0] = sa_q_cw; c5.cb[0] = sa_q_cb; c5.mode[0] = 0;
@@ -619,36 +604,32 @@
     c5.in[4] = preVca; c5.out[4] = VNca; c5.cw[4] = ca_v_cw; c5.cb[4] = ca_v_cb; c5.mode[4] = 1;
     conv5_kernel<<<dim3(512, 5), blk, 0, stream>>>(c5);
 
-    qk_softmax_kernel<<<dim3(4, 64), blk, 0, stream>>>(QT, KT, qk1o, PB, qscale);
-    gemm_mfma<1, 64><<<dim3(4, 64), blk, 0, stream>>>(PB, VNsa, ATTT, 256, 64, 256,
-        524288, 65536, kFW, 16384, kFW, 64, 3, 256, 256, 512, 1.0f);
-    WB5 so;
+    attn_kernel<<<dim3(4, 64), blk, 0, stream>>>(QT, KT, VNsa, qk1o, ATTT, qscale);
+    WB8 so;
     so.s[0] = { sa_o_pw, ATTT, saTb, 2 };
-    so.s[1] = so.s[0]; so.s[2] = so.s[0]; so.s[3] = so.s[0]; so.s[4] = so.s[0];
+    for (int i = 1; i < 8; ++i) so.s[i] = so.s[0];
     wgemm256<<<dim3(64), blk, 0, stream>>>(so, 512, 512, 512, 262144, kFW, kFW, 0, 8, 8, 1);
 
-    WB5 cq;
-    cq.s[0] = { ca_q_pw, CAT24, PRE16, 2 };
-    cq.s[1] = cq.s[0]; cq.s[2] = cq.s[0]; cq.s[3] = cq.s[0]; cq.s[4] = cq.s[0];
-    wgemm256<<<dim3(128), blk, 0, stream>>>(cq, 512, 512, 512, 262144, kFW, kFW, 0, 8, 8, 1);
+    WB8 cq2;
+    cq2.s[0] = { ca_q_pw + 8 * 262144, saTb, PRE16 + 8 * (size_t)kFW, 2 };
+    for (int i = 1; i < 8; ++i) cq2.s[i] = cq2.s[0];
+    wgemm256<<<dim3(64), blk, 0, stream>>>(cq2, 512, 512, 512, 262144, kFW, kFW, 0, 8, 8, 1);
     mixconv_kernel<<<512, blk, 0, stream>>>(PRE16, ca_q_dw, ca_q_cw, ca_q_cb, QTca);
 
-    qk_softmax_kernel<<<dim3(4, 64), blk, 0, stream>>>(QTca, KTca, qk2o, PB, qscale);
-    gemm_mfma<1, 64><<<dim3(4, 64), blk, 0, stream>>>(PB, VNca, ATTT, 256, 64, 256,
-        524288, 65536, kFW, 16384, kFW, 64, 3, 256, 256, 512, 1.0f);
-    WB5 co;
+    attn_kernel<<<dim3(4, 64), blk, 0, stream>>>(QTca, KTca, VNca, qk2o, ATTT, qscale);
+    WB8 co;
     co.s[0] = { ca_o_pw, ATTT, caTb, 2 };
-    co.s[1] = co.s[0]; co.s[2] = co.s[0]; co.s[3] = co.s[0]; co.s[4] = co.s[0];
+    for (int i = 1; i < 8; ++i) co.s[i] = co.s[0];
     wgemm256<<<dim3(64), blk, 0, stream>>>(co, 512, 512, 512, 262144, kFW, kFW, 0, 8, 8, 1);
 
-    WB5 f1;
+    WB8 f1;
     f1.s[0] = { ffn1_pw, CAT24, Z0T, 2 };
-    f1.s[1] = f1.s[0]; f1.s[2] = f1.s[0]; f1.s[3] = f1.s[0]; f1.s[4] = f1.s[0];
+    for (int i = 1; i < 8; ++i) f1.s[i] = f1.s[0];
     wgemm256<<<dim3(768), blk, 0, stream>>>(f1, 2048, 512, 512, 1048576, kFW, 524288, 0, 8, 32, 1);
     gelu24_kernel<<<2048, blk, 0, stream>>>(Z0T, ffn1_dw);
-    WB5 f2;
+    WB8 f2;
     f2.s[0] = { ffn2_pw, Z0T, Z2P, 0 };
-    f2.s[1] = f2.s[0]; f2.s[2] = f2.s[0]; f2.s[3] = f2.s[0]; f2.s[4] = f2.s[0];
+    for (int i = 1; i < 8; ++i) f2.s[i] = f2.s[0];
     wgemm256<<<dim3(384), blk, 0, stream>>>(f2, 512, 2048, 1024, 1048576, 524288, kFW, 3145728, 8, 8, 2);
     final_mix_add2<<<512, blk, 0, stream>>>(x, Z2P, ffn2_dw, out);
 }
```

Measured after the change: 295.8 us. 2.6% more time.
